# Kernel tuning notes

Hardware: AMD Instinct MI355X
Metric: run time of the kernel (lower is better)

## Reference

```python
import jax, jax.numpy as jnp
import numpy as np

EMB = 300
L = 5
N = 100000
E = 400000
G = 4000
ATOM_DIMS = np.array([119, 4, 12, 12, 10, 6, 6, 2, 2])
BOND_DIMS = np.array([5, 6, 2])
ATOM_OFF = jnp.asarray(np.concatenate([[0], np.cumsum(ATOM_DIMS)[:-1]]))
BOND_OFF = jnp.asarray(np.concatenate([[0], np.cumsum(BOND_DIMS)[:-1]]))
BN_EPS = 1e-5


def setup_inputs() -> dict:
    key = jax.random.key(0)
    ks = jax.random.split(key, 16)
    x = jax.random.randint(ks[0], (N, 9), 0, 2, dtype=jnp.int64)
    edge_index = jax.random.randint(ks[1], (2, E), 0, N, dtype=jnp.int64)
    edge_attr = jax.random.randint(ks[2], (E, 3), 0, 2, dtype=jnp.int64)
    batch = jnp.sort(jax.random.randint(ks[3], (N,), 0, G, dtype=jnp.int64))
    s = 0.05
    atom_emb = jax.random.normal(ks[4], (int(ATOM_DIMS.sum()), EMB), jnp.float32) * s
    bond_emb = jax.random.normal(ks[5], (int(BOND_DIMS.sum()), EMB), jnp.float32) * s
    W1 = jax.random.normal(ks[6], (L, EMB, 2 * EMB), jnp.float32) * (1.0 / np.sqrt(EMB))
    b1 = jnp.zeros((L, 2 * EMB), jnp.float32)
    g1 = jnp.ones((L, 2 * EMB), jnp.float32)
    bt1 = jnp.zeros((L, 2 * EMB), jnp.float32)
    W2 = jax.random.normal(ks[7], (L, 2 * EMB, EMB), jnp.float32) * (1.0 / np.sqrt(2 * EMB))
    b2 = jnp.zeros((L, EMB), jnp.float32)
    g2 = jnp.ones((L, EMB), jnp.float32)
    bt2 = jnp.zeros((L, EMB), jnp.float32)
    return dict(x=x, edge_index=edge_index, edge_attr=edge_attr, batch=batch,
                atom_emb=atom_emb, bond_emb=bond_emb,
                W1=W1, b1=b1, g1=g1, bt1=bt1, W2=W2, b2=b2, g2=g2, bt2=bt2)


def _bn(h, g, b):
    # BatchNorm1d, training-mode forward (batch stats, biased var)
    m = h.mean(0)
    v = h.var(0)
    return (h - m) * jax.lax.rsqrt(v + BN_EPS) * g + b


def reference(x, edge_index, edge_attr, batch, atom_emb, bond_emb,
              W1, b1, g1, bt1, W2, b2, g2, bt2):
    src, dst = edge_index[0], edge_index[1]
    # AtomEncoder / BondEncoder: sum of per-feature embeddings
    h = atom_emb[x + ATOM_OFF[None, :]].sum(axis=1)          # [N, EMB]
    ea = bond_emb[edge_attr + BOND_OFF[None, :]].sum(axis=1)  # [E, EMB]
    for i in range(L):
        # GINEConv: aggr = sum_j relu(x_j + e_ij); out = mlp((1+eps)*x + aggr), eps=0
        msg = jax.nn.relu(h[src] + ea)                        # [E, EMB]
        agg = jax.ops.segment_sum(msg, dst, num_segments=N)   # [N, EMB]
        z = h + agg
        z = _bn(z @ W1[i] + b1[i], g1[i], bt1[i])             # [N, 2*EMB]
        z = jax.nn.relu(z)
        h = z @ W2[i] + b2[i]                                 # [N, EMB]
        h = _bn(h, g2[i], bt2[i])
        if i != L - 1:
            h = jax.nn.relu(h)
        # dropout with p=0.0 is identity
    return jax.ops.segment_sum(h, batch, num_segments=G)      # [G, EMB]
```

## Files before the change

kernel.cpp:

```cpp
#include <hip/hip_runtime.h>

#define NN 100000
#define EE 400000
#define GG 4000
#define EMB 300
#define EMB2 600
#define LL 5
#define BN_EPS 1e-5f
#define BUF_BYTES 120000000ull
#define SCAN_NB 98
#define WSET 1597440ull

#define BAR_LGKM() asm volatile("s_waitcnt lgkmcnt(0)\ns_barrier" ::: "memory")

typedef __attribute__((ext_vector_type(8))) short bf16x8;
typedef __attribute__((ext_vector_type(4))) short bf16x4;
typedef __attribute__((ext_vector_type(2))) short bf16x2;
typedef __attribute__((ext_vector_type(4))) float f32x4;

__device__ __constant__ int c_atom_off[9] = {0,119,123,135,147,157,163,169,171};

static __device__ __forceinline__ float u16tof(unsigned short u) {
    return __uint_as_float(((unsigned int)u) << 16);
}
static __device__ __forceinline__ unsigned short ftobf(float f) {
    unsigned int u = __float_as_uint(f);
    unsigned int r = 0x7fffu + ((u >> 16) & 1u);
    return (unsigned short)((u + r) >> 16);
}
static __device__ __forceinline__ int geti(const void* p, int f64, long long i) {
    return f64 ? (int)((const long long*)p)[i] : ((const int*)p)[i];
}
static __device__ __forceinline__ f32x4 mfma16(bf16x8 a, bf16x8 b, f32x4 c) {
    return __builtin_amdgcn_mfma_f32_16x16x32_bf16(a, b, c, 0, 0, 0);
}

__global__ void k_detect(const int* __restrict__ ei, int* __restrict__ flag) {
    __shared__ int cnt;
    if (threadIdx.x == 0) cnt = 0;
    __syncthreads();
    int z = 0;
    for (int i = threadIdx.x; i < 1024; i += 256)
        if (ei[2 * i + 1] == 0) z++;
    atomicAdd(&cnt, z);
    __syncthreads();
    if (threadIdx.x == 0) *flag = (cnt > 512) ? 1 : 0;
}

__global__ void k_init(float* __restrict__ sc2, float* __restrict__ sh2) {
    const int c = blockIdx.x * 256 + threadIdx.x;
    if (c < EMB) { sc2[c] = 1.f; sh2[c] = 0.f; }
}

__global__ void k_encode(const void* __restrict__ x, const float* __restrict__ aemb,
                         float* __restrict__ h, const int* __restrict__ flag) {
    __shared__ int xi[4][9];
    const int ty = threadIdx.y, tx = threadIdx.x;
    const int n = blockIdx.x * 4 + ty;
    const int f64 = *flag;
    if (tx < 9) xi[ty][tx] = geti(x, f64, (long long)n * 9 + tx) + c_atom_off[tx];
    __syncthreads();
    if (tx < 75) {
        const int c = tx * 4;
        float s0 = 0.f, s1 = 0.f, s2 = 0.f, s3 = 0.f;
#pragma unroll
        for (int f = 0; f < 9; ++f) {
            const float4 v = *(const float4*)(aemb + (size_t)xi[ty][f] * EMB + c);
            s0 += v.x; s1 += v.y; s2 += v.z; s3 += v.w;
        }
        float4 o; o.x = s0; o.y = s1; o.z = s2; o.w = s3;
        *(float4*)(h + (size_t)n * EMB + c) = o;
    }
}

__global__ void k_deg(const void* __restrict__ ei, int* __restrict__ deg,
                      const int* __restrict__ flag) {
    const int e = blockIdx.x * 256 + threadIdx.x;
    if (e < EE) atomicAdd(&deg[geti(ei, *flag, (long long)EE + e)], 1);
}

__global__ void k_scanA(const int* __restrict__ deg, int* __restrict__ bsum) {
    __shared__ int red[256];
    const int b = blockIdx.x, t = threadIdx.x;
    const int base = b * 1024 + t * 4;
    int s = 0;
#pragma unroll
    for (int e = 0; e < 4; ++e) {
        const int i = base + e;
        if (i < NN) s += deg[i];
    }
    red[t] = s;
    __syncthreads();
    for (int off = 128; off > 0; off >>= 1) {
        if (t < off) red[t] += red[t + off];
        __syncthreads();
    }
    if (t == 0) bsum[b] = red[0];
}

__global__ void k_scanB(const int* __restrict__ bsum, int* __restrict__ bbase,
                        int* __restrict__ rowstart) {
    if (threadIdx.x == 0) {
        int run = 0;
        for (int b = 0; b < SCAN_NB; ++b) { bbase[b] = run; run += bsum[b]; }
        rowstart[NN] = run;
    }
}

__global__ void k_scanC(const int* __restrict__ deg, const int* __restrict__ bbase,
                        int* __restrict__ rowstart, int* __restrict__ cursor) {
    __shared__ int ts[256];
    const int b = blockIdx.x, t = threadIdx.x;
    const int base = b * 1024 + t * 4;
    int loc[4];
    int s = 0;
#pragma unroll
    for (int e = 0; e < 4; ++e) {
        const int i = base + e;
        loc[e] = (i < NN) ? deg[i] : 0;
        s += loc[e];
    }
    ts[t] = s;
    __syncthreads();
    for (int off = 1; off < 256; off <<= 1) {
        const int v = (t >= off) ? ts[t - off] : 0;
        __syncthreads();
        ts[t] += v;
        __syncthreads();
    }
    int run = bbase[b] + ts[t] - s;
#pragma unroll
    for (int e = 0; e < 4; ++e) {
        const int i = base + e;
        if (i < NN) { rowstart[i] = run; cursor[i] = run; run += loc[e]; }
    }
}

__global__ void k_scatter(const void* __restrict__ ei, const void* __restrict__ eattr,
                          int* __restrict__ cursor, int* __restrict__ elist,
                          const int* __restrict__ flag) {
    const int e = blockIdx.x * 256 + threadIdx.x;
    if (e >= EE) return;
    const int f64 = *flag;
    const int src = geti(ei, f64, e);
    const int dst = geti(ei, f64, (long long)EE + e);
    const int b0 = geti(eattr, f64, (long long)e * 3 + 0);
    const int b1 = geti(eattr, f64, (long long)e * 3 + 1);
    const int b2 = geti(eattr, f64, (long long)e * 3 + 2);
    const int pos = atomicAdd(&cursor[dst], 1);
    elist[pos] = src * 64 + b0 * 12 + b1 * 2 + b2;
}

__global__ void k_ebc(const float* __restrict__ bemb, float* __restrict__ ebc) {
    const int cb = blockIdx.x;
    const int tx = threadIdx.x;
    if (tx >= 75) return;
    const int b0 = cb / 12, b1 = (cb / 2) % 6, b2 = cb & 1;
    const int c = tx * 4;
    const float4 v0 = *(const float4*)(bemb + (size_t)b0 * EMB + c);
    const float4 v1 = *(const float4*)(bemb + (size_t)(5 + b1) * EMB + c);
    const float4 v2 = *(const float4*)(bemb + (size_t)(11 + b2) * EMB + c);
    float4 o; o.x = v0.x + v1.x + v2.x; o.y = v0.y + v1.y + v2.y;
    o.z = v0.z + v1.z + v2.z; o.w = v0.w + v1.w + v2.w;
    *(float4*)(ebc + (size_t)cb * EMB + c) = o;
}

__global__ void k_gather(const int* __restrict__ rowstart, const int* __restrict__ elist,
                         const float* __restrict__ ebc,
                         const float* __restrict__ h, float* __restrict__ z,
                         const float* __restrict__ sc, const float* __restrict__ sh,
                         int dorelu) {
    const int ty = threadIdx.y, tx = threadIdx.x;
    const int n = blockIdx.x * 4 + ty;
    if (tx >= 75) return;
    const int c = tx * 4;
    const float4 s4 = *(const float4*)(sc + c);
    const float4 h4 = *(const float4*)(sh + c);
    const int s = rowstart[n], e = rowstart[n + 1];
    float4 acc;
    {
        float4 v = *(const float4*)(h + (size_t)n * EMB + c);
        v.x = fmaf(v.x, s4.x, h4.x); v.y = fmaf(v.y, s4.y, h4.y);
        v.z = fmaf(v.z, s4.z, h4.z); v.w = fmaf(v.w, s4.w, h4.w);
        if (dorelu) {
            v.x = fmaxf(v.x, 0.f); v.y = fmaxf(v.y, 0.f);
            v.z = fmaxf(v.z, 0.f); v.w = fmaxf(v.w, 0.f);
        }
        acc = v;
    }
    for (int j = s; j < e; j += 4) {
        const int m = e - j;
        int pk[4];
#pragma unroll
        for (int d = 0; d < 4; ++d) pk[d] = (d < m) ? elist[j + d] : 0;
        float4 hv[4], ev[4];
#pragma unroll
        for (int d = 0; d < 4; ++d) {
            if (d < m) {
                const int src = pk[d] >> 6, cb = pk[d] & 63;
                hv[d] = *(const float4*)(h + (size_t)src * EMB + c);
                ev[d] = *(const float4*)(ebc + (size_t)cb * EMB + c);
            }
        }
#pragma unroll
        for (int d = 0; d < 4; ++d) {
            if (d < m) {
                float4 t = hv[d];
                t.x = fmaf(t.x, s4.x, h4.x); t.y = fmaf(t.y, s4.y, h4.y);
                t.z = fmaf(t.z, s4.z, h4.z); t.w = fmaf(t.w, s4.w, h4.w);
                if (dorelu) {
                    t.x = fmaxf(t.x, 0.f); t.y = fmaxf(t.y, 0.f);
                    t.z = fmaxf(t.z, 0.f); t.w = fmaxf(t.w, 0.f);
                }
                acc.x += fmaxf(t.x + ev[d].x, 0.f);
                acc.y += fmaxf(t.y + ev[d].y, 0.f);
                acc.z += fmaxf(t.z + ev[d].z, 0.f);
                acc.w += fmaxf(t.w + ev[d].w, 0.f);
            }
        }
    }
    *(float4*)(z + (size_t)n * EMB + c) = acc;
}

__global__ void k_wconv1(const float* __restrict__ W, unsigned short* __restrict__ hi,
                         unsigned short* __restrict__ lo) {
    const int idx = blockIdx.x * 256 + threadIdx.x;
    if (idx >= 10 * 40 * 64 * 8) return;
    const int e = idx & 7;
    const int lane = (idx >> 3) & 63;
    const int nt = (idx >> 9) % 40;
    const int kt = idx / 20480;
    const int r = lane & 15, g = lane >> 4;
    const int col = nt * 16 + r;
    const int k = kt * 32 + g * 8 + e;
    const float w = (col < EMB2 && k < EMB) ? W[(size_t)k * EMB2 + col] : 0.f;
    const unsigned short h = ftobf(w);
    hi[idx] = h;
    lo[idx] = ftobf(w - u16tof(h));
}
__global__ void k_wconv2(const float* __restrict__ W, unsigned short* __restrict__ hi,
                         unsigned short* __restrict__ lo) {
    const int idx = blockIdx.x * 256 + threadIdx.x;
    if (idx >= 19 * 20 * 64 * 8) return;
    const int e = idx & 7;
    const int lane = (idx >> 3) & 63;
    const int nt = (idx >> 9) % 20;
    const int kt = idx / 10240;
    const int r = lane & 15, g = lane >> 4;
    const int col = nt * 16 + r;
    const int k = kt * 32 + g * 8 + e;
    const float w = (col < EMB && k < EMB2) ? W[(size_t)k * EMB + col] : 0.f;
    const unsigned short h = ftobf(w);
    hi[idx] = h;
    lo[idx] = ftobf(w - u16tof(h));
}

__global__ __launch_bounds__(512) void k_mfma1(
    float* __restrict__ P, float* Q,
    const unsigned short* __restrict__ whi, const unsigned short* __restrict__ wlo)
{
    __shared__ __align__(16) short AsH[3][1024];
    __shared__ __align__(16) short AsL[3][1024];
    const int tid = threadIdx.x;
    const int lane = tid & 63;
    const int wn = tid >> 6;
    const int g = lane >> 4, r = lane & 15;
    const int row0 = blockIdx.x * 32;
    const int se2 = (tid & 3) * 2, str = (tid >> 2) & 15, stg = (tid >> 6) & 3, srg = tid >> 8;
    const int srow = row0 + srg * 16 + str;
    const int sldo = tid * 2;
    f32x4 acc[2][5];
#pragma unroll
    for (int rg = 0; rg < 2; ++rg)
#pragma unroll
        for (int t = 0; t < 5; ++t) acc[rg][t] = (f32x4){0.f, 0.f, 0.f, 0.f};

    auto loadA = [&](int kt, float2& v) {
        const int cc = kt * 32 + stg * 8 + se2;
        v = (float2){0.f, 0.f};
        if (cc + 1 < EMB) v = *(const float2*)(Q + (size_t)srow * EMB + cc);
    };
    auto writeA = [&](int b, float2 v) {
        bf16x2 h2, l2;
        const unsigned short hx = ftobf(v.x);
        h2[0] = (short)hx; l2[0] = (short)ftobf(v.x - u16tof(hx));
        const unsigned short hy = ftobf(v.y);
        h2[1] = (short)hy; l2[1] = (short)ftobf(v.y - u16tof(hy));
        *(bf16x2*)(&AsH[b][sldo]) = h2;
        *(bf16x2*)(&AsL[b][sldo]) = l2;
    };

    {
        float2 v0;
        loadA(0, v0);
        writeA(0, v0);
    }
    float2 vpend;
    loadA(1, vpend);
    BAR_LGKM();

    for (int kt = 0; kt < 10; ++kt) {
        const int cur = kt - (kt / 3) * 3;
        float2 vnext = {0.f, 0.f};
        if (kt + 2 < 10) loadA(kt + 2, vnext);
        bf16x8 ah[2], al[2];
#pragma unroll
        for (int rg = 0; rg < 2; ++rg) {
            ah[rg] = *(const bf16x8*)(&AsH[cur][rg * 512 + lane * 8]);
            al[rg] = *(const bf16x8*)(&AsL[cur][rg * 512 + lane * 8]);
        }
#pragma unroll
        for (int t = 0; t < 5; ++t) {
            const size_t wb = ((size_t)(kt * 40 + wn + t * 8) * 64 + lane) * 8;
            const bf16x8 bh = *(const bf16x8*)(whi + wb);
            const bf16x8 bl = *(const bf16x8*)(wlo + wb);
#pragma unroll
            for (int rg = 0; rg < 2; ++rg) {
                acc[rg][t] = mfma16(al[rg], bh, acc[rg][t]);
                acc[rg][t] = mfma16(ah[rg], bl, acc[rg][t]);
                acc[rg][t] = mfma16(ah[rg], bh, acc[rg][t]);
            }
        }
        if (kt + 1 < 10) {
            const int nb = (kt + 1) - ((kt + 1) / 3) * 3;
            writeA(nb, vpend);
        }
        vpend = vnext;
        BAR_LGKM();
    }
#pragma unroll
    for (int t = 0; t < 5; ++t) {
        const int col = (wn + t * 8) * 16 + r;
#pragma unroll
        for (int rg = 0; rg < 2; ++rg) {
            const int orow = row0 + rg * 16 + g * 4;
#pragma unroll
            for (int j = 0; j < 4; ++j) {
                const float val = acc[rg][t][j];
                if (col < EMB)       Q[(size_t)(orow + j) * EMB + col] = val;
                else if (col < EMB2) P[(size_t)(orow + j) * EMB + (col - EMB)] = val;
            }
        }
    }
}

__global__ __launch_bounds__(256) void k_mfma2(
    float* P, const float* __restrict__ Qa,
    const float* __restrict__ sc, const float* __restrict__ sh,
    const unsigned short* __restrict__ whi, const unsigned short* __restrict__ wlo)
{
    __shared__ __align__(16) short AsH[3][1024];
    __shared__ __align__(16) short AsL[3][1024];
    const int tid = threadIdx.x;
    const int lane = tid & 63;
    const int wn = tid >> 6;
    const int g = lane >> 4, r = lane & 15;
    const int row0 = blockIdx.x * 32;
    const int se4 = (tid & 1) * 4, str = (tid >> 1) & 15, stg = (tid >> 5) & 3, srg = tid >> 7;
    const int srow = row0 + srg * 16 + str;
    const int sldo = tid * 4;
    f32x4 acc[2][5];
#pragma unroll
    for (int rg = 0; rg < 2; ++rg)
#pragma unroll
        for (int t = 0; t < 5; ++t) acc[rg][t] = (f32x4){0.f, 0.f, 0.f, 0.f};

    auto loadA = [&](int kt, float4& v) {
        const int cc = kt * 32 + stg * 8 + se4;
        v = (float4){0.f, 0.f, 0.f, 0.f};
        if (cc + 3 < EMB)       v = *(const float4*)(Qa + (size_t)srow * EMB + cc);
        else if (cc + 3 < EMB2) v = *(const float4*)(P + (size_t)srow * EMB + (cc - EMB));
    };
    auto writeA = [&](int kt, int b, float4 v) {
        const int cc = kt * 32 + stg * 8 + se4;
        if (cc + 3 < EMB2) {
            const float4 s4 = *(const float4*)(sc + cc);
            const float4 h4 = *(const float4*)(sh + cc);
            v.x = fmaxf(fmaf(v.x, s4.x, h4.x), 0.f);
            v.y = fmaxf(fmaf(v.y, s4.y, h4.y), 0.f);
            v.z = fmaxf(fmaf(v.z, s4.z, h4.z), 0.f);
            v.w = fmaxf(fmaf(v.w, s4.w, h4.w), 0.f);
        } else {
            v = (float4){0.f, 0.f, 0.f, 0.f};
        }
        bf16x4 h4v, l4v;
        const float vv[4] = {v.x, v.y, v.z, v.w};
#pragma unroll
        for (int e = 0; e < 4; ++e) {
            const unsigned short hh = ftobf(vv[e]);
            h4v[e] = (short)hh;
            l4v[e] = (short)ftobf(vv[e] - u16tof(hh));
        }
        *(bf16x4*)(&AsH[b][sldo]) = h4v;
        *(bf16x4*)(&AsL[b][sldo]) = l4v;
    };

    {
        float4 v0;
        loadA(0, v0);
        writeA(0, 0, v0);
    }
    float4 vpend;
    loadA(1, vpend);
    BAR_LGKM();

    for (int kt = 0; kt < 19; ++kt) {
        const int cur = kt - (kt / 3) * 3;
        float4 vnext = {0.f, 0.f, 0.f, 0.f};
        if (kt + 2 < 19) loadA(kt + 2, vnext);
        bf16x8 ah[2], al[2];
#pragma unroll
        for (int rg = 0; rg < 2; ++rg) {
            ah[rg] = *(const bf16x8*)(&AsH[cur][rg * 512 + lane * 8]);
            al[rg] = *(const bf16x8*)(&AsL[cur][rg * 512 + lane * 8]);
        }
#pragma unroll
        for (int t = 0; t < 5; ++t) {
            const size_t wb = ((size_t)(kt * 20 + wn + t * 4) * 64 + lane) * 8;
            const bf16x8 bh = *(const bf16x8*)(whi + wb);
            const bf16x8 bl = *(const bf16x8*)(wlo + wb);
#pragma unroll
            for (int rg = 0; rg < 2; ++rg) {
                acc[rg][t] = mfma16(al[rg], bh, acc[rg][t]);
                acc[rg][t] = mfma16(ah[rg], bl, acc[rg][t]);
                acc[rg][t] = mfma16(ah[rg], bh, acc[rg][t]);
            }
        }
        if (kt + 1 < 19) {
            const int nb = (kt + 1) - ((kt + 1) / 3) * 3;
            writeA(kt + 1, nb, vpend);
        }
        vpend = vnext;
        BAR_LGKM();
    }
#pragma unroll
    for (int t = 0; t < 5; ++t) {
        const int col = (wn + t * 4) * 16 + r;
        if (col < EMB) {
#pragma unroll
            for (int rg = 0; rg < 2; ++rg) {
                const int orow = row0 + rg * 16 + g * 4;
#pragma unroll
                for (int j = 0; j < 4; ++j)
                    P[(size_t)(orow + j) * EMB + col] = acc[rg][t][j];
            }
        }
    }
}

__global__ void k_statsz(const float* __restrict__ Qm, const float* __restrict__ Pm,
                         float* __restrict__ sum, float* __restrict__ ss) {
    const int c = blockIdx.x * 256 + threadIdx.x;
    if (c >= EMB2) return;
    const float* m = (c < EMB) ? Qm : Pm;
    const int cc = (c < EMB) ? c : c - EMB;
    const int r0 = blockIdx.y * 250;
    const int r1 = r0 + 250;
    float s = 0.f, q = 0.f;
    for (int r = r0; r < r1; ++r) {
        const float v = m[(size_t)r * EMB + cc];
        s += v; q += v * v;
    }
    atomicAdd(&sum[c], s);
    atomicAdd(&ss[c], q);
}

__global__ void k_stats(const float* __restrict__ m, float* __restrict__ sum, float* __restrict__ ss) {
    const int c = blockIdx.x * 256 + threadIdx.x;
    if (c >= EMB) return;
    const int r0 = blockIdx.y * 200;
    const int r1 = r0 + 200;
    float s = 0.f, q = 0.f;
    for (int r = r0; r < r1; ++r) {
        const float v = m[(size_t)r * EMB + c];
        s += v; q += v * v;
    }
    atomicAdd(&sum[c], s);
    atomicAdd(&ss[c], q);
}

__global__ void k_scale(const float* __restrict__ sum, const float* __restrict__ ss,
                        const float* __restrict__ g, const float* __restrict__ b,
                        float* __restrict__ scale, float* __restrict__ shift, int C) {
    const int c = blockIdx.x * 256 + threadIdx.x;
    if (c >= C) return;
    const float invN = 1.0f / (float)NN;
    const float mean = sum[c] * invN;
    const float var = ss[c] * invN - mean * mean;
    const float s = g[c] * rsqrtf(var + BN_EPS);
    scale[c] = s;
    shift[c] = b[c] - mean * s;
}

__global__ void k_poolg(const void* __restrict__ batch, const float* __restrict__ h,
                        float* __restrict__ out, const int* __restrict__ flag,
                        const float* __restrict__ sc, const float* __restrict__ sh) {
    __shared__ float red[4][EMB];
    const int g = blockIdx.x;
    const int f64 = *flag;
    int lo = 0, hi = NN;
    while (lo < hi) { int mid = (lo + hi) >> 1; if (geti(batch, f64, mid) < g) lo = mid + 1; else hi = mid; }
    const int s = lo;
    hi = NN;
    while (lo < hi) { int mid = (lo + hi) >> 1; if (geti(batch, f64, mid) < g + 1) lo = mid + 1; else hi = mid; }
    const int e = lo;
    const int tx = threadIdx.x, ty = threadIdx.y;
    if (tx < 75) {
        const int c = tx * 4;
        const float4 s4 = *(const float4*)(sc + c);
        const float4 h4 = *(const float4*)(sh + c);
        float4 acc; acc.x = acc.y = acc.z = acc.w = 0.f;
        int cntr = 0;
        for (int r = s + ty; r < e; r += 4) {
            const float4 v = *(const float4*)(h + (size_t)r * EMB + c);
            acc.x += v.x; acc.y += v.y; acc.z += v.z; acc.w += v.w;
            cntr++;
        }
        acc.x = fmaf(acc.x, s4.x, cntr * h4.x);
        acc.y = fmaf(acc.y, s4.y, cntr * h4.y);
        acc.z = fmaf(acc.z, s4.z, cntr * h4.z);
        acc.w = fmaf(acc.w, s4.w, cntr * h4.w);
        *(float4*)(&red[ty][c]) = acc;
    }
    __syncthreads();
    if (ty == 0 && tx < 75) {
        const int c = tx * 4;
        float4 o;
        o.x = red[0][c + 0] + red[1][c + 0] + red[2][c + 0] + red[3][c + 0];
        o.y = red[0][c + 1] + red[1][c + 1] + red[2][c + 1] + red[3][c + 1];
        o.z = red[0][c + 2] + red[1][c + 2] + red[2][c + 2] + red[3][c + 2];
        o.w = red[0][c + 3] + red[1][c + 3] + red[2][c + 3] + red[3][c + 3];
        *(float4*)(out + (size_t)g * EMB + c) = o;
    }
}

extern "C" void kernel_launch(void* const* d_in, const int* in_sizes, int n_in,
                              void* d_out, int out_size, void* d_ws, size_t ws_size,
                              hipStream_t stream) {
    const void* x     = d_in[0];
    const void* ei    = d_in[1];
    const void* eattr = d_in[2];
    const void* batch = d_in[3];
    const float* aemb = (const float*)d_in[4];
    const float* bemb = (const float*)d_in[5];
    const float* W1   = (const float*)d_in[6];
    const float* g1   = (const float*)d_in[8];
    const float* bt1  = (const float*)d_in[9];
    const float* W2   = (const float*)d_in[10];
    const float* g2   = (const float*)d_in[12];
    const float* bt2  = (const float*)d_in[13];

    char* ws = (char*)d_ws;
    const bool pre2 = (ws_size >= 2ull * BUF_BYTES + 2888640ull + 5ull * WSET);

    float* P = (float*)(ws);
    float* Q = (float*)(ws + BUF_BYTES);
    char* aux = ws + 2ull * BUF_BYTES;

    float* st = (float*)(aux);
    float* sum1 = st;         float* ss1 = st + 600;
    float* sum2 = st + 1200;  float* ss2 = st + 1500;
    float* sc1  = st + 1800;  float* sh1 = st + 2400;
    float* sc2  = st + 3000;  float* sh2 = st + 3300;
    int* flag     = (int*)(aux + 16384);
    int* deg      = (int*)(aux + 16384 + 64);
    int* rowstart = (int*)(aux + 16384 + 64 + 400064);
    int* cursor   = (int*)(aux + 16384 + 64 + 800128);
    int* elist    = (int*)(aux + 16384 + 64 + 1200192);
    float* ebc    = (float*)(aux + 16384 + 64 + 2800192);
    int* bsum     = (int*)(aux + 2872192);
    int* bbase    = (int*)(aux + 2872192 + 512);
    char* wbase   = aux + 2888640;

    const dim3 blk80x4(80, 4);

    k_detect<<<1, 256, 0, stream>>>((const int*)ei, flag);
    k_init<<<2, 256, 0, stream>>>(sc2, sh2);

    (void)hipMemsetAsync(deg, 0, NN * sizeof(int), stream);
    k_deg<<<(EE + 255) / 256, 256, 0, stream>>>(ei, deg, flag);
    k_scanA<<<SCAN_NB, 256, 0, stream>>>(deg, bsum);
    k_scanB<<<1, 64, 0, stream>>>(bsum, bbase, rowstart);
    k_scanC<<<SCAN_NB, 256, 0, stream>>>(deg, bbase, rowstart, cursor);
    k_scatter<<<(EE + 255) / 256, 256, 0, stream>>>(ei, eattr, cursor, elist, flag);
    k_ebc<<<60, 80, 0, stream>>>(bemb, ebc);

    if (pre2) {
        for (int i = 0; i < LL; ++i) {
            char* wb = wbase + (size_t)i * WSET;
            k_wconv1<<<(204800 + 255) / 256, 256, 0, stream>>>(
                W1 + (size_t)i * EMB * EMB2,
                (unsigned short*)wb, (unsigned short*)(wb + 409600));
            k_wconv2<<<(194560 + 255) / 256, 256, 0, stream>>>(
                W2 + (size_t)i * EMB2 * EMB,
                (unsigned short*)(wb + 819200), (unsigned short*)(wb + 819200 + 389120));
        }
    }

    k_encode<<<NN / 4, blk80x4, 0, stream>>>(x, aemb, P, flag);

    for (int i = 0; i < LL; ++i) {
        char* wb = wbase + (pre2 ? (size_t)i * WSET : 0ull);
        unsigned short* wt1hi = (unsigned short*)wb;
        unsigned short* wt1lo = (unsigned short*)(wb + 409600);
        unsigned short* wt2hi = (unsigned short*)(wb + 819200);
        unsigned short* wt2lo = (unsigned short*)(wb + 819200 + 389120);

        if (!pre2) {
            k_wconv1<<<(204800 + 255) / 256, 256, 0, stream>>>(
                W1 + (size_t)i * EMB * EMB2, wt1hi, wt1lo);
            k_wconv2<<<(194560 + 255) / 256, 256, 0, stream>>>(
                W2 + (size_t)i * EMB2 * EMB, wt2hi, wt2lo);
        }
        (void)hipMemsetAsync(st, 0, 1800 * sizeof(float), stream);

        k_gather<<<NN / 4, blk80x4, 0, stream>>>(rowstart, elist, ebc, P, Q,
                                                 sc2, sh2, (i > 0) ? 1 : 0);
        k_mfma1<<<NN / 32, 512, 0, stream>>>(P, Q, wt1hi, wt1lo);

        k_statsz<<<dim3(3, 400), 256, 0, stream>>>(Q, P, sum1, ss1);
        k_scale<<<3, 256, 0, stream>>>(sum1, ss1, g1 + (size_t)i * EMB2,
                                       bt1 + (size_t)i * EMB2, sc1, sh1, EMB2);

        k_mfma2<<<NN / 32, 256, 0, stream>>>(P, Q, sc1, sh1, wt2hi, wt2lo);

        k_stats<<<dim3(2, 500), 256, 0, stream>>>(P, sum2, ss2);
        k_scale<<<2, 256, 0, stream>>>(sum2, ss2, g2 + (size_t)i * EMB,
                                       bt2 + (size_t)i * EMB, sc2, sh2, EMB);
    }

    k_poolg<<<GG, blk80x4, 0, stream>>>(batch, P, (float*)d_out, flag, sc2, sh2);
}
```

Baseline: 3.027 ms.

## Process two K-tiles per barrier in second MFMA GEMM with 4-slot LDS ring

Restructures the k_mfma2 main loop to consume two 32-wide K tiles between barriers, using a 4-slot LDS ring buffer and prefetching two tiles further ahead in registers. This halves the number of block barriers and gives more global-load latency hiding. It costs more LDS and more registers for the extra prefetched float4s, which could affect occupancy.

```diff
diff --git a/kernel.cpp b/kernel.cpp
--- a/kernel.cpp
+++ b/kernel.cpp
@@ -349,8 +349,8 @@
     const float* __restrict__ sc, const float* __restrict__ sh,
     const unsigned short* __restrict__ whi, const unsigned short* __restrict__ wlo)
 {
-    __shared__ __align__(16) short AsH[3][1024];
-    __shared__ __align__(16) short AsL[3][1024];
+    __shared__ __align__(16) short AsH[4][1024];
+    __shared__ __align__(16) short AsL[4][1024];
     const int tid = threadIdx.x;
     const int lane = tid & 63;
     const int wn = tid >> 6;
@@ -394,25 +394,12 @@
         *(bf16x4*)(&AsH[b][sldo]) = h4v;
         *(bf16x4*)(&AsL[b][sldo]) = l4v;
     };
-
-    {
-        float4 v0;
-        loadA(0, v0);
-        writeA(0, 0, v0);
-    }
-    float4 vpend;
-    loadA(1, vpend);
-    BAR_LGKM();
-
-    for (int kt = 0; kt < 19; ++kt) {
-        const int cur = kt - (kt / 3) * 3;
-        float4 vnext = {0.f, 0.f, 0.f, 0.f};
-        if (kt + 2 < 19) loadA(kt + 2, vnext);
+    auto consume = [&](int kt, int slot) {
         bf16x8 ah[2], al[2];
 #pragma unroll
         for (int rg = 0; rg < 2; ++rg) {
-            ah[rg] = *(const bf16x8*)(&AsH[cur][rg * 512 + lane * 8]);
-            al[rg] = *(const bf16x8*)(&AsL[cur][rg * 512 + lane * 8]);
+            ah[rg] = *(const bf16x8*)(&AsH[slot][rg * 512 + lane * 8]);
+            al[rg] = *(const bf16x8*)(&AsL[slot][rg * 512 + lane * 8]);
         }
 #pragma unroll
         for (int t = 0; t < 5; ++t) {
@@ -426,11 +413,27 @@
                 acc[rg][t] = mfma16(ah[rg], bh, acc[rg][t]);
             }
         }
-        if (kt + 1 < 19) {
-            const int nb = (kt + 1) - ((kt + 1) / 3) * 3;
-            writeA(kt + 1, nb, vpend);
-        }
-        vpend = vnext;
+    };
+
+    {
+        float4 v0, v1;
+        loadA(0, v0); writeA(0, 0, v0);
+        loadA(1, v1); writeA(1, 1, v1);
+    }
+    float4 p0, p1;
+    loadA(2, p0);
+    loadA(3, p1);
+    BAR_LGKM();
+
+    for (int kt = 0; kt < 19; kt += 2) {
+        float4 n0 = {0.f, 0.f, 0.f, 0.f}, n1 = {0.f, 0.f, 0.f, 0.f};
+        if (kt + 4 < 19) loadA(kt + 4, n0);
+        if (kt + 5 < 19) loadA(kt + 5, n1);
+        consume(kt, kt & 3);
+        if (kt + 1 < 19) consume(kt + 1, (kt + 1) & 3);
+        if (kt + 2 < 19) writeA(kt + 2, (kt + 2) & 3, p0);
+        if (kt + 3 < 19) writeA(kt + 3, (kt + 3) & 3, p1);
+        p0 = n0; p1 = n1;
         BAR_LGKM();
     }
 #pragma unroll
```

Measured after the change: 3.049 ms. Within noise of the previous version (+0.7%).

## Fuse BatchNorm column statistics into MFMA GEMM epilogues with striped partial sums

Applied to the files above, without the earlier changes.

Computes per-column sum and sum-of-squares in the epilogues of both GEMM kernels, reducing across lanes with shuffles and atomically adding into 16 striped partial-sum copies. The separate stats kernels, which re-read the full activation matrices from memory, are removed, and a new scale kernel sums the 16 copies. The partial buffers reuse the cursor region of the workspace, which risks aliasing if that region is still needed. Float atomics also make the statistics order-nondeterministic.

```diff
diff --git a/kernel.cpp b/kernel.cpp
--- a/kernel.cpp
+++ b/kernel.cpp
@@ -10,6 +10,7 @@
 #define BUF_BYTES 120000000ull
 #define SCAN_NB 98
 #define WSET 1597440ull
+#define NCOPY 16
 
 #define BAR_LGKM() asm volatile("s_waitcnt lgkmcnt(0)\ns_barrier" ::: "memory")
 
@@ -257,7 +258,8 @@
 
 __global__ __launch_bounds__(512) void k_mfma1(
     float* __restrict__ P, float* Q,
-    const unsigned short* __restrict__ whi, const unsigned short* __restrict__ wlo)
+    const unsigned short* __restrict__ whi, const unsigned short* __restrict__ wlo,
+    float* __restrict__ sum1p, float* __restrict__ ss1p)
 {
     __shared__ __align__(16) short AsH[3][1024];
     __shared__ __align__(16) short AsL[3][1024];
@@ -266,6 +268,7 @@
     const int wn = tid >> 6;
     const int g = lane >> 4, r = lane & 15;
     const int row0 = blockIdx.x * 32;
+    const int cp = (blockIdx.x & (NCOPY - 1)) * EMB2;
     const int se2 = (tid & 3) * 2, str = (tid >> 2) & 15, stg = (tid >> 6) & 3, srg = tid >> 8;
     const int srow = row0 + srg * 16 + str;
     const int sldo = tid * 2;
@@ -331,23 +334,32 @@
 #pragma unroll
     for (int t = 0; t < 5; ++t) {
         const int col = (wn + t * 8) * 16 + r;
+        float s = 0.f, q = 0.f;
 #pragma unroll
         for (int rg = 0; rg < 2; ++rg) {
             const int orow = row0 + rg * 16 + g * 4;
 #pragma unroll
             for (int j = 0; j < 4; ++j) {
                 const float val = acc[rg][t][j];
+                s += val; q += val * val;
                 if (col < EMB)       Q[(size_t)(orow + j) * EMB + col] = val;
                 else if (col < EMB2) P[(size_t)(orow + j) * EMB + (col - EMB)] = val;
             }
         }
+        s += __shfl_xor(s, 16); s += __shfl_xor(s, 32);
+        q += __shfl_xor(q, 16); q += __shfl_xor(q, 32);
+        if (g == 0 && col < EMB2) {
+            atomicAdd(&sum1p[cp + col], s);
+            atomicAdd(&ss1p[cp + col], q);
+        }
     }
 }
 
 __global__ __launch_bounds__(256) void k_mfma2(
     float* P, const float* __restrict__ Qa,
     const float* __restrict__ sc, const float* __restrict__ sh,
-    const unsigned short* __restrict__ whi, const unsigned short* __restrict__ wlo)
+    const unsigned short* __restrict__ whi, const unsigned short* __restrict__ wlo,
+    float* __restrict__ sum2p, float* __restrict__ ss2p)
 {
     __shared__ __align__(16) short AsH[3][1024];
     __shared__ __align__(16) short AsL[3][1024];
@@ -356,6 +368,7 @@
     const int wn = tid >> 6;
     const int g = lane >> 4, r = lane & 15;
     const int row0 = blockIdx.x * 32;
+    const int cp = (blockIdx.x & (NCOPY - 1)) * EMB;
     const int se4 = (tid & 1) * 4, str = (tid >> 1) & 15, stg = (tid >> 5) & 3, srg = tid >> 7;
     const int srow = row0 + srg * 16 + str;
     const int sldo = tid * 4;
@@ -436,60 +449,43 @@
 #pragma unroll
     for (int t = 0; t < 5; ++t) {
         const int col = (wn + t * 4) * 16 + r;
-        if (col < EMB) {
-#pragma unroll
-            for (int rg = 0; rg < 2; ++rg) {
-                const int orow = row0 + rg * 16 + g * 4;
-#pragma unroll
-                for (int j = 0; j < 4; ++j)
-                    P[(size_t)(orow + j) * EMB + col] = acc[rg][t][j];
+        float s = 0.f, q = 0.f;
+#pragma unroll
+        for (int rg = 0; rg < 2; ++rg) {
+            const int orow = row0 + rg * 16 + g * 4;
+#pragma unroll
+            for (int j = 0; j < 4; ++j) {
+                const float val = acc[rg][t][j];
+                s += val; q += val * val;
+                if (col < EMB) P[(size_t)(orow + j) * EMB + col] = val;
             }
         }
-    }
-}
-
-__global__ void k_statsz(const float* __restrict__ Qm, const float* __restrict__ Pm,
-                         float* __restrict__ sum, float* __restrict__ ss) {
-    const int c = blockIdx.x * 256 + threadIdx.x;
-    if (c >= EMB2) return;
-    const float* m = (c < EMB) ? Qm : Pm;
-    const int cc = (c < EMB) ? c : c - EMB;
-    const int r0 = blockIdx.y * 250;
-    const int r1 = r0 + 250;
-    float s = 0.f, q = 0.f;
-    for (int r = r0; r < r1; ++r) {
-        const float v = m[(size_t)r * EMB + cc];
-        s += v; q += v * v;
-    }
-    atomicAdd(&sum[c], s);
-    atomicAdd(&ss[c], q);
-}
-
-__global__ void k_stats(const float* __restrict__ m, float* __restrict__ sum, float* __restrict__ ss) {
-    const int c = blockIdx.x * 256 + threadIdx.x;
-    if (c >= EMB) return;
-    const int r0 = blockIdx.y * 200;
-    const int r1 = r0 + 200;
-    float s = 0.f, q = 0.f;
-    for (int r = r0; r < r1; ++r) {
-        const float v = m[(size_t)r * EMB + c];
-        s += v; q += v * v;
-    }
-    atomicAdd(&sum[c], s);
-    atomicAdd(&ss[c], q);
-}
-
-__global__ void k_scale(const float* __restrict__ sum, const float* __restrict__ ss,
-                        const float* __restrict__ g, const float* __restrict__ b,
-                        float* __restrict__ scale, float* __restrict__ shift, int C) {
+        s += __shfl_xor(s, 16); s += __shfl_xor(s, 32);
+        q += __shfl_xor(q, 16); q += __shfl_xor(q, 32);
+        if (g == 0 && col < EMB) {
+            atomicAdd(&sum2p[cp + col], s);
+            atomicAdd(&ss2p[cp + col], q);
+        }
+    }
+}
+
+__global__ void k_scale16(const float* __restrict__ psum, const float* __restrict__ pss,
+                          const float* __restrict__ g, const float* __restrict__ b,
+                          float* __restrict__ scale, float* __restrict__ shift, int C) {
     const int c = blockIdx.x * 256 + threadIdx.x;
     if (c >= C) return;
+    float s = 0.f, q = 0.f;
+#pragma unroll
+    for (int k = 0; k < NCOPY; ++k) {
+        s += psum[k * C + c];
+        q += pss[k * C + c];
+    }
     const float invN = 1.0f / (float)NN;
-    const float mean = sum[c] * invN;
-    const float var = ss[c] * invN - mean * mean;
-    const float s = g[c] * rsqrtf(var + BN_EPS);
-    scale[c] = s;
-    shift[c] = b[c] - mean * s;
+    const float mean = s * invN;
+    const float var = q * invN - mean * mean;
+    const float sc = g[c] * rsqrtf(var + BN_EPS);
+    scale[c] = sc;
+    shift[c] = b[c] - mean * sc;
 }
 
 __global__ void k_poolg(const void* __restrict__ batch, const float* __restrict__ h,
@@ -558,8 +554,6 @@
     char* aux = ws + 2ull * BUF_BYTES;
 
     float* st = (float*)(aux);
-    float* sum1 = st;         float* ss1 = st + 600;
-    float* sum2 = st + 1200;  float* ss2 = st + 1500;
     float* sc1  = st + 1800;  float* sh1 = st + 2400;
     float* sc2  = st + 3000;  float* sh2 = st + 3300;
     int* flag     = (int*)(aux + 16384);
@@ -571,6 +565,11 @@
     int* bsum     = (int*)(aux + 2872192);
     int* bbase    = (int*)(aux + 2872192 + 512);
     char* wbase   = aux + 2888640;
+    float* parts  = (float*)cursor;
+    float* sum1p  = parts;
+    float* ss1p   = parts + 9600;
+    float* sum2p  = parts + 19200;
+    float* ss2p   = parts + 24000;
 
     const dim3 blk80x4(80, 4);
 
@@ -612,21 +611,18 @@
             k_wconv2<<<(194560 + 255) / 256, 256, 0, stream>>>(
                 W2 + (size_t)i * EMB2 * EMB, wt2hi, wt2lo);
         }
-        (void)hipMemsetAsync(st, 0, 1800 * sizeof(float), stream);
+        (void)hipMemsetAsync(parts, 0, 28800 * sizeof(float), stream);
 
         k_gather<<<NN / 4, blk80x4, 0, stream>>>(rowstart, elist, ebc, P, Q,
                                                  sc2, sh2, (i > 0) ? 1 : 0);
-        k_mfma1<<<NN / 32, 512, 0, stream>>>(P, Q, wt1hi, wt1lo);
-
-        k_statsz<<<dim3(3, 400), 256, 0, stream>>>(Q, P, sum1, ss1);
-        k_scale<<<3, 256, 0, stream>>>(sum1, ss1, g1 + (size_t)i * EMB2,
-                                       bt1 + (size_t)i * EMB2, sc1, sh1, EMB2);
-
-        k_mfma2<<<NN / 32, 256, 0, stream>>>(P, Q, sc1, sh1, wt2hi, wt2lo);
-
-        k_stats<<<dim3(2, 500), 256, 0, stream>>>(P, sum2, ss2);
-        k_scale<<<2, 256, 0, stream>>>(sum2, ss2, g2 + (size_t)i * EMB,
-                                       bt2 + (size_t)i * EMB, sc2, sh2, EMB);
+
+        k_mfma1<<<NN / 32, 512, 0, stream>>>(P, Q, wt1hi, wt1lo, sum1p, ss1p);
+        k_scale16<<<3, 256, 0, stream>>>(sum1p, ss1p, g1 + (size_t)i * EMB2,
+                                         bt1 + (size_t)i * EMB2, sc1, sh1, EMB2);
+
+        k_mfma2<<<NN / 32, 256, 0, stream>>>(P, Q, sc1, sh1, wt2hi, wt2lo, sum2p, ss2p);
+        k_scale16<<<2, 256, 0, stream>>>(sum2p, ss2p, g2 + (size_t)i * EMB,
+                                         bt2 + (size_t)i * EMB, sc2, sh2, EMB);
     }
 
     k_poolg<<<GG, blk80x4, 0, stream>>>(batch, P, (float*)d_out, flag, sc2, sh2);
```

Measured after the change: 2.673 ms (median of 2 runs). 11.7% less time.
